# Optimization experiments

Hardware: AMD Instinct MI355X
Metric: run time of the kernel (lower is better)

The kernel has to match this reference:

```python
import jax, jax.numpy as jnp
import numpy as np

B, T, D = 64, 4096, 100   # batch, tokens, token_dim == code_dim
K = 4                     # discrete_size: codebook entries
BETA = 0.25               # commitment loss weight


def setup_inputs() -> dict:
    key = jax.random.key(0)
    k_x, k_w, k_b, k_c = jax.random.split(key, 4)
    x = jax.random.normal(k_x, (B, T, D), dtype=jnp.float32)
    W1 = jax.random.normal(k_w, (D, D), dtype=jnp.float32) * (1.0 / np.sqrt(D))
    b1 = jax.random.normal(k_b, (D,), dtype=jnp.float32) * 0.01
    codebook = jax.random.normal(k_c, (K, D), dtype=jnp.float32)
    return {"x": x, "W1": W1, "b1": b1, "codebook": codebook, "quantize": 1}


def reference(x, W1, b1, codebook, quantize):
    # Linear1: Linear(100,100) + ReLU (torch Linear: x @ W.T + b)
    h = jax.nn.relu(jnp.einsum("btd,ed->bte", x, W1) + b1)  # [B,T,D]
    if not quantize:
        return (h, 0, 0, 0)
    # quantizer.compress: VQ-style cdist/argmin/straight-through/loss
    flat = h.reshape(-1, D)  # [N,D]
    d2 = (jnp.sum(flat * flat, axis=-1, keepdims=True)
          - 2.0 * flat @ codebook.T
          + jnp.sum(codebook * codebook, axis=-1))
    idx = jnp.argmin(d2, axis=-1)          # [N] nearest code indices
    q = codebook[idx]                       # [N,D] gathered codes
    sg = jax.lax.stop_gradient
    # codebook loss + commitment loss
    vq_loss = (jnp.mean((sg(flat) - q) ** 2)
               + BETA * jnp.mean((flat - sg(q)) ** 2))
    # straight-through quantized output
    aux = (flat + sg(q - flat)).reshape(B, T, D)
    payload = idx.reshape(B, T)
    return (h, payload, aux, vq_loss)
```

## Files before the change

### kernel.cpp

```cpp
#include <hip/hip_runtime.h>

#define D_DIM   100
#define K_CODES 4
#define RPB     64
#define TPB     256
#define PITCH   65
#define N_ROWS  262144
#define KP      128
#define NP      128
#define TAU     0.25

typedef __attribute__((ext_vector_type(8))) __bf16 bf16x8;
typedef __attribute__((ext_vector_type(4))) float  f32x4;

__device__ __forceinline__ unsigned short f2bf_rne(float f) {
    unsigned int u = __builtin_bit_cast(unsigned int, f);
    unsigned int r = u + 0x7fffu + ((u >> 16) & 1u);
    return (unsigned short)(r >> 16);
}
__device__ __forceinline__ float bf2f(unsigned short b) {
    unsigned int u = ((unsigned int)b) << 16;
    return __builtin_bit_cast(float, u);
}

__global__ __launch_bounds__(256) void split_w_kernel(
    const float* __restrict__ W1,
    unsigned short* __restrict__ Whi, unsigned short* __restrict__ Wlo)
{
    int i = blockIdx.x * 256 + threadIdx.x;
    if (i >= NP * KP) return;
    int n = i / KP, k = i % KP;
    float w = (n < D_DIM && k < D_DIM) ? W1[n * D_DIM + k] : 0.0f;
    unsigned short hb = f2bf_rne(w);
    float lo = w - bf2f(hb);
    Whi[i] = hb;
    Wlo[i] = f2bf_rne(lo);
}

__global__ __launch_bounds__(TPB) void gemm_relu_mfma(
    const float* __restrict__ x,
    const unsigned short* __restrict__ Whi, const unsigned short* __restrict__ Wlo,
    const float* __restrict__ b1, float* __restrict__ out_h)
{
    __shared__ unsigned short xhi[RPB * KP];
    __shared__ unsigned short xlo[RPB * KP];
    const int tid  = threadIdx.x;
    const int lane = tid & 63;
    const int wave = tid >> 6;
    const int rowBase = blockIdx.x * RPB;
    const float* xg = x + (size_t)rowBase * D_DIM;

    const int bcol0 = wave * 32;
    const int bn  = lane & 15;
    const int bk  = (lane >> 4) * 8;
    bf16x8 bh[2][4], bl[2][4];
    #pragma unroll
    for (int ct = 0; ct < 2; ++ct) {
        int n = bcol0 + ct * 16 + bn;
        #pragma unroll
        for (int kt = 0; kt < 4; ++kt) {
            int off = n * KP + kt * 32 + bk;
            bh[ct][kt] = *reinterpret_cast<const bf16x8*>(Whi + off);
            bl[ct][kt] = *reinterpret_cast<const bf16x8*>(Wlo + off);
        }
    }
    float bias[2];
    #pragma unroll
    for (int ct = 0; ct < 2; ++ct) {
        int n = bcol0 + ct * 16 + bn;
        bias[ct] = (n < D_DIM) ? b1[n] : 0.0f;
    }

    for (int v = tid; v < RPB * 25; v += TPB) {
        float4 val = reinterpret_cast<const float4*>(xg)[v];
        int r = v / 25;
        int d = (v % 25) * 4;
        ushort4 hw, lw;
        hw.x = f2bf_rne(val.x); lw.x = f2bf_rne(val.x - bf2f(hw.x));
        hw.y = f2bf_rne(val.y); lw.y = f2bf_rne(val.y - bf2f(hw.y));
        hw.z = f2bf_rne(val.z); lw.z = f2bf_rne(val.z - bf2f(hw.z));
        hw.w = f2bf_rne(val.w); lw.w = f2bf_rne(val.w - bf2f(hw.w));
        int byte = r * 256 + ((d * 2) ^ ((r & 7) << 4));
        *reinterpret_cast<ushort4*>(reinterpret_cast<char*>(xhi) + byte) = hw;
        *reinterpret_cast<ushort4*>(reinterpret_cast<char*>(xlo) + byte) = lw;
    }
    for (int v = tid; v < RPB * 7; v += TPB) {
        int r = v / 7;
        int c = v % 7;
        int byte = r * 256 + (((200 + c * 8)) ^ ((r & 7) << 4));
        ushort4 z = {0, 0, 0, 0};
        *reinterpret_cast<ushort4*>(reinterpret_cast<char*>(xhi) + byte) = z;
        *reinterpret_cast<ushort4*>(reinterpret_cast<char*>(xlo) + byte) = z;
    }
    __syncthreads();

    const int am = lane & 15;
    const int ak = (lane >> 4) * 8;
    #pragma unroll
    for (int rt = 0; rt < 4; ++rt) {
        const int mrow = rt * 16 + am;
        bf16x8 ah[4], al[4];
        #pragma unroll
        for (int kt = 0; kt < 4; ++kt) {
            int byte = mrow * 256 + (((kt * 32 + ak) * 2) ^ ((mrow & 7) << 4));
            ah[kt] = *reinterpret_cast<const bf16x8*>(reinterpret_cast<const char*>(xhi) + byte);
            al[kt] = *reinterpret_cast<const bf16x8*>(reinterpret_cast<const char*>(xlo) + byte);
        }
        #pragma unroll
        for (int ct = 0; ct < 2; ++ct) {
            f32x4 acc = {0.f, 0.f, 0.f, 0.f};
            #pragma unroll
            for (int kt = 0; kt < 4; ++kt) {
                acc = __builtin_amdgcn_mfma_f32_16x16x32_bf16(ah[kt], bl[ct][kt], acc, 0, 0, 0);
                acc = __builtin_amdgcn_mfma_f32_16x16x32_bf16(al[kt], bh[ct][kt], acc, 0, 0, 0);
                acc = __builtin_amdgcn_mfma_f32_16x16x32_bf16(ah[kt], bh[ct][kt], acc, 0, 0, 0);
            }
            int n = bcol0 + ct * 16 + bn;
            if (n < D_DIM) {
                int rb = rt * 16 + (lane >> 4) * 4;
                #pragma unroll
                for (int i = 0; i < 4; ++i) {
                    float h = fmaxf(acc[i] + bias[ct], 0.0f);
                    out_h[(size_t)(rowBase + rb + i) * D_DIM + n] = h;
                }
            }
        }
    }
}

__global__ __launch_bounds__(TPB) void gemm_relu_valu(
    const float* __restrict__ x, const float* __restrict__ W1,
    const float* __restrict__ b1, float* __restrict__ out_h)
{
    __shared__ float tile[D_DIM][PITCH];
    const int tid  = threadIdx.x;
    const int lane = tid & 63;
    const int wave = tid >> 6;
    const int rowBase = blockIdx.x * RPB;
    const float* xg = x + (size_t)rowBase * D_DIM;

    for (int v = tid; v < (RPB * D_DIM) / 4; v += TPB) {
        float4 val = reinterpret_cast<const float4*>(xg)[v];
        int r = v / 25;
        int d = (v % 25) * 4;
        tile[d + 0][r] = val.x; tile[d + 1][r] = val.y;
        tile[d + 2][r] = val.z; tile[d + 3][r] = val.w;
    }
    __syncthreads();
    const int e0 = __builtin_amdgcn_readfirstlane(wave * 25);
    float acc[25];
    #pragma unroll
    for (int j = 0; j < 25; ++j) acc[j] = b1[e0 + j];
    #pragma unroll
    for (int d0 = 0; d0 < D_DIM; d0 += 20) {
        float xv[20];
        #pragma unroll
        for (int dd = 0; dd < 20; ++dd) xv[dd] = tile[d0 + dd][lane];
        #pragma unroll
        for (int j = 0; j < 25; ++j) {
            const float* wr = W1 + (e0 + j) * D_DIM + d0;
            #pragma unroll
            for (int dd = 0; dd < 20; ++dd)
                acc[j] = fmaf(xv[dd], wr[dd], acc[j]);
        }
    }
    __syncthreads();
    #pragma unroll
    for (int j = 0; j < 25; ++j)
        tile[e0 + j][lane] = fmaxf(acc[j], 0.0f);
    __syncthreads();
    float* hg = out_h + (size_t)rowBase * D_DIM;
    for (int v = tid; v < (RPB * D_DIM) / 4; v += TPB) {
        int r = v / 25;
        int d = (v % 25) * 4;
        reinterpret_cast<float4*>(hg)[v] =
            make_float4(tile[d][r], tile[d+1][r], tile[d+2][r], tile[d+3][r]);
    }
}

__global__ __launch_bounds__(TPB) void vq_kernel(
    const float* __restrict__ h, const float* __restrict__ x,
    const float* __restrict__ W1, const float* __restrict__ b1,
    const float* __restrict__ cb, const int* __restrict__ qflag,
    float* __restrict__ out_pay, float* __restrict__ out_aux,
    double* __restrict__ partials)
{
    __shared__ float  tile[D_DIM][PITCH];
    __shared__ double d2s[K_CODES][RPB];
    __shared__ int    idxs[RPB];
    __shared__ unsigned long long flagmask;
    const int tid  = threadIdx.x;
    const int lane = tid & 63;
    const int wave = tid >> 6;
    const int blk  = blockIdx.x;
    const int rowBase = blk * RPB;
    const int qz = *qflag;

    if (qz) {
        const float* hgc = h + (size_t)rowBase * D_DIM;
        for (int v = tid; v < (RPB * D_DIM) / 4; v += TPB) {
            float4 val = reinterpret_cast<const float4*>(hgc)[v];
            int r = v / 25;
            int d = (v % 25) * 4;
            tile[d + 0][r] = val.x; tile[d + 1][r] = val.y;
            tile[d + 2][r] = val.z; tile[d + 3][r] = val.w;
        }
        __syncthreads();
        {
            const int k = __builtin_amdgcn_readfirstlane(wave & 3);
            const float* crow = cb + k * D_DIM;
            double s = 0.0;
            #pragma unroll
            for (int d = 0; d < D_DIM; ++d) {
                double dh = (double)tile[d][lane] - (double)crow[d];
                s = fma(dh, dh, s);
            }
            d2s[k][lane] = s;
        }
        __syncthreads();

        if (wave == 0) {
            double best = d2s[0][lane], second = 1e300;
            int bi = 0;
            #pragma unroll
            for (int k = 1; k < K_CODES; ++k) {
                double v = d2s[k][lane];
                if (v < best) { second = best; best = v; bi = k; }
                else if (v < second) { second = v; }
            }
            idxs[lane] = bi;
            unsigned long long m = __ballot((second - best) < TAU);
            if (lane == 0) flagmask = m;
        }
        __syncthreads();

        {
            unsigned long long m = flagmask;
            int i = 0;
            while (m) {
                int r = __ffsll((long long)m) - 1;
                m &= m - 1;
                if ((i & 3) == wave) {
                    const int e1 = lane;
                    const int e2 = 64 + lane;
                    const bool has2 = (e2 < D_DIM);
                    float z1 = b1[e1];
                    float z2 = has2 ? b1[e2] : 0.0f;
                    const float* xr  = x + (size_t)(rowBase + r) * D_DIM;
                    const float* w1r = W1 + e1 * D_DIM;
                    const float* w2r = W1 + (has2 ? e2 : 0) * D_DIM;
                    #pragma unroll
                    for (int d4 = 0; d4 < 25; ++d4) {
                        float4 xv = reinterpret_cast<const float4*>(xr)[d4];
                        float4 wa = reinterpret_cast<const float4*>(w1r)[d4];
                        z1 = fmaf(xv.x, wa.x, z1); z1 = fmaf(xv.y, wa.y, z1);
                        z1 = fmaf(xv.z, wa.z, z1); z1 = fmaf(xv.w, wa.w, z1);
                        float4 wb = reinterpret_cast<const float4*>(w2r)[d4];
                        z2 = fmaf(xv.x, wb.x, z2); z2 = fmaf(xv.y, wb.y, z2);
                        z2 = fmaf(xv.z, wb.z, z2); z2 = fmaf(xv.w, wb.w, z2);
                    }
                    float h1 = fmaxf(z1, 0.0f);
                    float h2 = fmaxf(z2, 0.0f);
                    double dk[K_CODES];
                    #pragma unroll
                    for (int k = 0; k < K_CODES; ++k) {
                        double p;
                        {
                            double dh = (double)h1 - (double)cb[k * D_DIM + e1];
                            p = dh * dh;
                        }
                        if (has2) {
                            double dh = (double)h2 - (double)cb[k * D_DIM + e2];
                            p = fma(dh, dh, p);
                        }
                        for (int off = 32; off > 0; off >>= 1)
                            p += __shfl_down(p, off);
                        dk[k] = p;
                    }
                    if (lane == 0) {
                        double best = dk[0];
                        int bi = 0;
                        #pragma unroll
                        for (int k = 1; k < K_CODES; ++k)
                            if (dk[k] < best) { best = dk[k]; bi = k; }
                        idxs[r] = bi;
                    }
                }
                ++i;
            }
        }
        __syncthreads();

        if (wave == 0) {
            int bi = idxs[lane];
            out_pay[rowBase + lane] = (float)bi;
            double d2min = d2s[bi][lane];
            for (int off = 32; off > 0; off >>= 1)
                d2min += __shfl_down(d2min, off);
            if (lane == 0) partials[blk] = d2min;
        }

        float* ag = out_aux + (size_t)rowBase * D_DIM;
        for (int v = tid; v < (RPB * D_DIM) / 4; v += TPB) {
            int r = v / 25;
            int d = (v % 25) * 4;
            int bi = idxs[r];
            reinterpret_cast<float4*>(ag)[v] =
                reinterpret_cast<const float4*>(cb + bi * D_DIM + d)[0];
        }
    } else {
        if (wave == 0) {
            out_pay[rowBase + lane] = 0.0f;
            if (lane == 0) partials[blk] = 0.0;
        }
        float* ag = out_aux + (size_t)rowBase * D_DIM;
        for (int v = tid; v < (RPB * D_DIM) / 4; v += TPB)
            reinterpret_cast<float4*>(ag)[v] = make_float4(0, 0, 0, 0);
    }
}

__global__ __launch_bounds__(256) void vq_final_kernel(
    const double* __restrict__ partials, int n, float* __restrict__ loss_out)
{
    __shared__ double sm[256];
    int tid = threadIdx.x;
    double s = 0.0;
    for (int i = tid; i < n; i += 256) s += partials[i];
    sm[tid] = s;
    __syncthreads();
    for (int off = 128; off > 0; off >>= 1) {
        if (tid < off) sm[tid] += sm[tid + off];
        __syncthreads();
    }
    if (tid == 0) {
        double mse = sm[0] / ((double)N_ROWS * (double)D_DIM);
        loss_out[0] = (float)(1.25 * mse);
    }
}

extern "C" void kernel_launch(void* const* d_in, const int* in_sizes, int n_in,
                              void* d_out, int out_size, void* d_ws, size_t ws_size,
                              hipStream_t stream) {
    const float* x  = (const float*)d_in[0];
    const float* W1 = (const float*)d_in[1];
    const float* b1 = (const float*)d_in[2];
    const float* cb = (const float*)d_in[3];
    const int* qflag = (const int*)d_in[4];

    float* out = (float*)d_out;
    const int NR = in_sizes[0] / D_DIM;
    const int nblocks = NR / RPB;

    float* out_h    = out;
    float* out_pay  = out + (size_t)NR * D_DIM;
    float* out_aux  = out_pay + NR;
    float* out_loss = out_aux + (size_t)NR * D_DIM;

    double* partials = (double*)d_ws;
    const size_t w_off = (size_t)nblocks * sizeof(double);
    unsigned short* Whi = (unsigned short*)((char*)d_ws + w_off);
    unsigned short* Wlo = Whi + NP * KP;
    const size_t need = w_off + (size_t)2 * NP * KP * sizeof(unsigned short);

    if (ws_size >= need) {
        split_w_kernel<<<(NP * KP) / 256, 256, 0, stream>>>(W1, Whi, Wlo);
        gemm_relu_mfma<<<nblocks, TPB, 0, stream>>>(x, Whi, Wlo, b1, out_h);
    } else {
        gemm_relu_valu<<<nblocks, TPB, 0, stream>>>(x, W1, b1, out_h);
    }
    vq_kernel<<<nblocks, TPB, 0, stream>>>(out_h, x, W1, b1, cb, qflag,
                                           out_pay, out_aux, partials);
    vq_final_kernel<<<1, 256, 0, stream>>>(partials, nblocks, out_loss);
}
```

Measured before the change: 145.1 us.

## Fuse MFMA GEMM+ReLU with VQ kernel, keeping h in shared memory

Merges the split-bf16 MFMA GEMM and the VQ distance/argmin kernel into one kernel. The ReLU output is staged in a transposed shared-memory tile that reuses the bf16 staging buffer, and the VQ stage reads it directly. This removes the global write-then-reread of h and one launch. The bf16 conversion now uses native casts, and the workspace-size fallback to the VALU GEMM is dropped, which risks failure if the workspace is too small.

```diff
diff --git a/kernel.cpp b/kernel.cpp
--- a/kernel.cpp
+++ b/kernel.cpp
@@ -37,18 +37,29 @@
     Wlo[i] = f2bf_rne(lo);
 }
 
-__global__ __launch_bounds__(TPB) void gemm_relu_mfma(
+__global__ __launch_bounds__(TPB) void fused_kernel(
     const float* __restrict__ x,
     const unsigned short* __restrict__ Whi, const unsigned short* __restrict__ Wlo,
-    const float* __restrict__ b1, float* __restrict__ out_h)
+    const float* __restrict__ b1, const float* __restrict__ cb,
+    const float* __restrict__ W1, const int* __restrict__ qflag,
+    float* __restrict__ out_h, float* __restrict__ out_pay,
+    float* __restrict__ out_aux, double* __restrict__ partials)
 {
-    __shared__ unsigned short xhi[RPB * KP];
-    __shared__ unsigned short xlo[RPB * KP];
+    __shared__ __align__(16) unsigned char smem[32768];
+    __shared__ double d2s[K_CODES][RPB];
+    __shared__ int    idxs[RPB];
+    __shared__ unsigned long long flagmask;
+    unsigned short* xhi = reinterpret_cast<unsigned short*>(smem);
+    unsigned short* xlo = xhi + RPB * KP;
+    float* ftile = reinterpret_cast<float*>(smem);
+
     const int tid  = threadIdx.x;
     const int lane = tid & 63;
     const int wave = tid >> 6;
-    const int rowBase = blockIdx.x * RPB;
+    const int blk  = blockIdx.x;
+    const int rowBase = blk * RPB;
     const float* xg = x + (size_t)rowBase * D_DIM;
+    const int qz = *qflag;
 
     const int bcol0 = wave * 32;
     const int bn  = lane & 15;
@@ -75,14 +86,22 @@
         float4 val = reinterpret_cast<const float4*>(xg)[v];
         int r = v / 25;
         int d = (v % 25) * 4;
-        ushort4 hw, lw;
-        hw.x = f2bf_rne(val.x); lw.x = f2bf_rne(val.x - bf2f(hw.x));
-        hw.y = f2bf_rne(val.y); lw.y = f2bf_rne(val.y - bf2f(hw.y));
-        hw.z = f2bf_rne(val.z); lw.z = f2bf_rne(val.z - bf2f(hw.z));
-        hw.w = f2bf_rne(val.w); lw.w = f2bf_rne(val.w - bf2f(hw.w));
+        __bf16 hx = (__bf16)val.x, hy = (__bf16)val.y,
+               hz = (__bf16)val.z, hw_ = (__bf16)val.w;
+        __bf16 lx = (__bf16)(val.x - (float)hx), ly = (__bf16)(val.y - (float)hy),
+               lz = (__bf16)(val.z - (float)hz), lw_ = (__bf16)(val.w - (float)hw_);
+        ushort4 hv, lv;
+        hv.x = __builtin_bit_cast(unsigned short, hx);
+        hv.y = __builtin_bit_cast(unsigned short, hy);
+        hv.z = __builtin_bit_cast(unsigned short, hz);
+        hv.w = __builtin_bit_cast(unsigned short, hw_);
+        lv.x = __builtin_bit_cast(unsigned short, lx);
+        lv.y = __builtin_bit_cast(unsigned short, ly);
+        lv.z = __builtin_bit_cast(unsigned short, lz);
+        lv.w = __builtin_bit_cast(unsigned short, lw_);
         int byte = r * 256 + ((d * 2) ^ ((r & 7) << 4));
-        *reinterpret_cast<ushort4*>(reinterpret_cast<char*>(xhi) + byte) = hw;
-        *reinterpret_cast<ushort4*>(reinterpret_cast<char*>(xlo) + byte) = lw;
+        *reinterpret_cast<ushort4*>(reinterpret_cast<char*>(xhi) + byte) = hv;
+        *reinterpret_cast<ushort4*>(reinterpret_cast<char*>(xlo) + byte) = lv;
     }
     for (int v = tid; v < RPB * 7; v += TPB) {
         int r = v / 7;
@@ -96,6 +115,7 @@
 
     const int am = lane & 15;
     const int ak = (lane >> 4) * 8;
+    f32x4 acc[4][2];
     #pragma unroll
     for (int rt = 0; rt < 4; ++rt) {
         const int mrow = rt * 16 + am;
@@ -108,111 +128,41 @@
         }
         #pragma unroll
         for (int ct = 0; ct < 2; ++ct) {
-            f32x4 acc = {0.f, 0.f, 0.f, 0.f};
+            f32x4 a = {0.f, 0.f, 0.f, 0.f};
             #pragma unroll
             for (int kt = 0; kt < 4; ++kt) {
-                acc = __builtin_amdgcn_mfma_f32_16x16x32_bf16(ah[kt], bl[ct][kt], acc, 0, 0, 0);
-                acc = __builtin_amdgcn_mfma_f32_16x16x32_bf16(al[kt], bh[ct][kt], acc, 0, 0, 0);
-                acc = __builtin_amdgcn_mfma_f32_16x16x32_bf16(ah[kt], bh[ct][kt], acc, 0, 0, 0);
-            }
+                a = __builtin_amdgcn_mfma_f32_16x16x32_bf16(ah[kt], bl[ct][kt], a, 0, 0, 0);
+                a = __builtin_amdgcn_mfma_f32_16x16x32_bf16(al[kt], bh[ct][kt], a, 0, 0, 0);
+                a = __builtin_amdgcn_mfma_f32_16x16x32_bf16(ah[kt], bh[ct][kt], a, 0, 0, 0);
+            }
+            acc[rt][ct] = a;
+        }
+    }
+    __syncthreads();
+
+    #pragma unroll
+    for (int rt = 0; rt < 4; ++rt) {
+        int rb = rt * 16 + (lane >> 4) * 4;
+        #pragma unroll
+        for (int ct = 0; ct < 2; ++ct) {
             int n = bcol0 + ct * 16 + bn;
             if (n < D_DIM) {
-                int rb = rt * 16 + (lane >> 4) * 4;
                 #pragma unroll
-                for (int i = 0; i < 4; ++i) {
-                    float h = fmaxf(acc[i] + bias[ct], 0.0f);
-                    out_h[(size_t)(rowBase + rb + i) * D_DIM + n] = h;
-                }
-            }
-        }
-    }
-}
-
-__global__ __launch_bounds__(TPB) void gemm_relu_valu(
-    const float* __restrict__ x, const float* __restrict__ W1,
-    const float* __restrict__ b1, float* __restrict__ out_h)
-{
-    __shared__ float tile[D_DIM][PITCH];
-    const int tid  = threadIdx.x;
-    const int lane = tid & 63;
-    const int wave = tid >> 6;
-    const int rowBase = blockIdx.x * RPB;
-    const float* xg = x + (size_t)rowBase * D_DIM;
-
-    for (int v = tid; v < (RPB * D_DIM) / 4; v += TPB) {
-        float4 val = reinterpret_cast<const float4*>(xg)[v];
-        int r = v / 25;
-        int d = (v % 25) * 4;
-        tile[d + 0][r] = val.x; tile[d + 1][r] = val.y;
-        tile[d + 2][r] = val.z; tile[d + 3][r] = val.w;
+                for (int i = 0; i < 4; ++i)
+                    ftile[n * PITCH + rb + i] = fmaxf(acc[rt][ct][i] + bias[ct], 0.0f);
+            }
+        }
     }
     __syncthreads();
-    const int e0 = __builtin_amdgcn_readfirstlane(wave * 25);
-    float acc[25];
-    #pragma unroll
-    for (int j = 0; j < 25; ++j) acc[j] = b1[e0 + j];
-    #pragma unroll
-    for (int d0 = 0; d0 < D_DIM; d0 += 20) {
-        float xv[20];
-        #pragma unroll
-        for (int dd = 0; dd < 20; ++dd) xv[dd] = tile[d0 + dd][lane];
-        #pragma unroll
-        for (int j = 0; j < 25; ++j) {
-            const float* wr = W1 + (e0 + j) * D_DIM + d0;
-            #pragma unroll
-            for (int dd = 0; dd < 20; ++dd)
-                acc[j] = fmaf(xv[dd], wr[dd], acc[j]);
-        }
-    }
-    __syncthreads();
-    #pragma unroll
-    for (int j = 0; j < 25; ++j)
-        tile[e0 + j][lane] = fmaxf(acc[j], 0.0f);
-    __syncthreads();
-    float* hg = out_h + (size_t)rowBase * D_DIM;
-    for (int v = tid; v < (RPB * D_DIM) / 4; v += TPB) {
-        int r = v / 25;
-        int d = (v % 25) * 4;
-        reinterpret_cast<float4*>(hg)[v] =
-            make_float4(tile[d][r], tile[d+1][r], tile[d+2][r], tile[d+3][r]);
-    }
-}
-
-__global__ __launch_bounds__(TPB) void vq_kernel(
-    const float* __restrict__ h, const float* __restrict__ x,
-    const float* __restrict__ W1, const float* __restrict__ b1,
-    const float* __restrict__ cb, const int* __restrict__ qflag,
-    float* __restrict__ out_pay, float* __restrict__ out_aux,
-    double* __restrict__ partials)
-{
-    __shared__ float  tile[D_DIM][PITCH];
-    __shared__ double d2s[K_CODES][RPB];
-    __shared__ int    idxs[RPB];
-    __shared__ unsigned long long flagmask;
-    const int tid  = threadIdx.x;
-    const int lane = tid & 63;
-    const int wave = tid >> 6;
-    const int blk  = blockIdx.x;
-    const int rowBase = blk * RPB;
-    const int qz = *qflag;
 
     if (qz) {
-        const float* hgc = h + (size_t)rowBase * D_DIM;
-        for (int v = tid; v < (RPB * D_DIM) / 4; v += TPB) {
-            float4 val = reinterpret_cast<const float4*>(hgc)[v];
-            int r = v / 25;
-            int d = (v % 25) * 4;
-            tile[d + 0][r] = val.x; tile[d + 1][r] = val.y;
-            tile[d + 2][r] = val.z; tile[d + 3][r] = val.w;
-        }
-        __syncthreads();
         {
             const int k = __builtin_amdgcn_readfirstlane(wave & 3);
             const float* crow = cb + k * D_DIM;
             double s = 0.0;
             #pragma unroll
             for (int d = 0; d < D_DIM; ++d) {
-                double dh = (double)tile[d][lane] - (double)crow[d];
+                double dh = (double)ftile[d * PITCH + lane] - (double)crow[d];
                 s = fma(dh, dh, s);
             }
             d2s[k][lane] = s;
@@ -300,10 +250,14 @@
             if (lane == 0) partials[blk] = d2min;
         }
 
+        float* hg = out_h + (size_t)rowBase * D_DIM;
         float* ag = out_aux + (size_t)rowBase * D_DIM;
-        for (int v = tid; v < (RPB * D_DIM) / 4; v += TPB) {
+        for (int v = tid; v < RPB * 25; v += TPB) {
             int r = v / 25;
             int d = (v % 25) * 4;
+            float4 hv = make_float4(ftile[d * PITCH + r], ftile[(d + 1) * PITCH + r],
+                                    ftile[(d + 2) * PITCH + r], ftile[(d + 3) * PITCH + r]);
+            reinterpret_cast<float4*>(hg)[v] = hv;
             int bi = idxs[r];
             reinterpret_cast<float4*>(ag)[v] =
                 reinterpret_cast<const float4*>(cb + bi * D_DIM + d)[0];
@@ -313,9 +267,16 @@
             out_pay[rowBase + lane] = 0.0f;
             if (lane == 0) partials[blk] = 0.0;
         }
+        float* hg = out_h + (size_t)rowBase * D_DIM;
         float* ag = out_aux + (size_t)rowBase * D_DIM;
-        for (int v = tid; v < (RPB * D_DIM) / 4; v += TPB)
+        for (int v = tid; v < RPB * 25; v += TPB) {
+            int r = v / 25;
+            int d = (v % 25) * 4;
+            float4 hv = make_float4(ftile[d * PITCH + r], ftile[(d + 1) * PITCH + r],
+                                    ftile[(d + 2) * PITCH + r], ftile[(d + 3) * PITCH + r]);
+            reinterpret_cast<float4*>(hg)[v] = hv;
             reinterpret_cast<float4*>(ag)[v] = make_float4(0, 0, 0, 0);
+        }
     }
 }
 
@@ -360,15 +321,9 @@
     const size_t w_off = (size_t)nblocks * sizeof(double);
     unsigned short* Whi = (unsigned short*)((char*)d_ws + w_off);
     unsigned short* Wlo = Whi + NP * KP;
-    const size_t need = w_off + (size_t)2 * NP * KP * sizeof(unsigned short);
-
-    if (ws_size >= need) {
-        split_w_kernel<<<(NP * KP) / 256, 256, 0, stream>>>(W1, Whi, Wlo);
-        gemm_relu_mfma<<<nblocks, TPB, 0, stream>>>(x, Whi, Wlo, b1, out_h);
-    } else {
-        gemm_relu_valu<<<nblocks, TPB, 0, stream>>>(x, W1, b1, out_h);
-    }
-    vq_kernel<<<nblocks, TPB, 0, stream>>>(out_h, x, W1, b1, cb, qflag,
-                                           out_pay, out_aux, partials);
+
+    split_w_kernel<<<(NP * KP) / 256, 256, 0, stream>>>(W1, Whi, Wlo);
+    fused_kernel<<<nblocks, TPB, 0, stream>>>(x, Whi, Wlo, b1, cb, W1, qflag,
+                                              out_h, out_pay, out_aux, partials);
     vq_final_kernel<<<1, 256, 0, stream>>>(partials, nblocks, out_loss);
 }
```

Measured after the change: 169.6 us. 1.17x slower.

## Stage x via direct global-to-LDS loads and coalesce h stores through shared memory

Applied to the files above, without the earlier changes.

The MFMA GEMM kernel now copies raw fp32 x tiles straight into LDS with global_load_lds instead of splitting them into bf16 hi/lo on the way in. The hi/lo split moves into the MFMA loop. Results are transposed through LDS so h is written with coalesced float4 stores rather than scattered scalar stores. It also adds an occupancy hint to the launch bounds and removes the VALU fallback path along with the workspace-size check. Risks include LDS bank conflicts from the unswizzled fp32 reads at a 100-float row stride, and no fallback if the workspace is too small.

```diff
diff --git a/kernel.cpp b/kernel.cpp
--- a/kernel.cpp
+++ b/kernel.cpp
@@ -21,6 +21,12 @@
 __device__ __forceinline__ float bf2f(unsigned short b) {
     unsigned int u = ((unsigned int)b) << 16;
     return __builtin_bit_cast(float, u);
+}
+
+__device__ __forceinline__ void load_lds16(const float* g, float* s) {
+    __builtin_amdgcn_global_load_lds(
+        (const __attribute__((address_space(1))) unsigned int*)g,
+        (__attribute__((address_space(3))) unsigned int*)s, 16, 0, 0);
 }
 
 __global__ __launch_bounds__(256) void split_w_kernel(
@@ -37,13 +43,12 @@
     Wlo[i] = f2bf_rne(lo);
 }
 
-__global__ __launch_bounds__(TPB) void gemm_relu_mfma(
+__global__ __launch_bounds__(TPB, 4) void gemm_relu_mfma(
     const float* __restrict__ x,
     const unsigned short* __restrict__ Whi, const unsigned short* __restrict__ Wlo,
     const float* __restrict__ b1, float* __restrict__ out_h)
 {
-    __shared__ unsigned short xhi[RPB * KP];
-    __shared__ unsigned short xlo[RPB * KP];
+    __shared__ __align__(16) float smem[6500];
     const int tid  = threadIdx.x;
     const int lane = tid & 63;
     const int wave = tid >> 6;
@@ -71,110 +76,76 @@
         bias[ct] = (n < D_DIM) ? b1[n] : 0.0f;
     }
 
+    #pragma unroll
+    for (int it = 0; it < 6; ++it) {
+        int cbase = it * 256 + wave * 64;
+        load_lds16(xg + (size_t)(cbase + lane) * 4, smem + cbase * 4);
+    }
+    if (wave == 0) {
+        int cbase = 1536;
+        load_lds16(xg + (size_t)(cbase + lane) * 4, smem + cbase * 4);
+    }
+    if (tid < 32) smem[6400 + tid] = 0.0f;
+    __syncthreads();
+
+    const int am = lane & 15;
+    const int ak = (lane >> 4) * 8;
+    f32x4 acc[4][2];
+    #pragma unroll
+    for (int rt = 0; rt < 4; ++rt) {
+        acc[rt][0] = (f32x4){0.f, 0.f, 0.f, 0.f};
+        acc[rt][1] = (f32x4){0.f, 0.f, 0.f, 0.f};
+    }
+    #pragma unroll
+    for (int rt = 0; rt < 4; ++rt) {
+        const int rbase = (rt * 16 + am) * D_DIM;
+        #pragma unroll
+        for (int kt = 0; kt < 4; ++kt) {
+            const float* p = smem + rbase + kt * 32 + ak;
+            f32x4 f0 = *reinterpret_cast<const f32x4*>(p);
+            f32x4 f1 = *reinterpret_cast<const f32x4*>(p + 4);
+            bf16x8 ah, al;
+            #pragma unroll
+            for (int i = 0; i < 4; ++i) {
+                __bf16 h0 = (__bf16)f0[i];
+                ah[i] = h0;
+                al[i] = (__bf16)(f0[i] - (float)h0);
+                __bf16 h1 = (__bf16)f1[i];
+                ah[4 + i] = h1;
+                al[4 + i] = (__bf16)(f1[i] - (float)h1);
+            }
+            acc[rt][0] = __builtin_amdgcn_mfma_f32_16x16x32_bf16(ah, bl[0][kt], acc[rt][0], 0, 0, 0);
+            acc[rt][0] = __builtin_amdgcn_mfma_f32_16x16x32_bf16(al, bh[0][kt], acc[rt][0], 0, 0, 0);
+            acc[rt][0] = __builtin_amdgcn_mfma_f32_16x16x32_bf16(ah, bh[0][kt], acc[rt][0], 0, 0, 0);
+            acc[rt][1] = __builtin_amdgcn_mfma_f32_16x16x32_bf16(ah, bl[1][kt], acc[rt][1], 0, 0, 0);
+            acc[rt][1] = __builtin_amdgcn_mfma_f32_16x16x32_bf16(al, bh[1][kt], acc[rt][1], 0, 0, 0);
+            acc[rt][1] = __builtin_amdgcn_mfma_f32_16x16x32_bf16(ah, bh[1][kt], acc[rt][1], 0, 0, 0);
+        }
+    }
+    __syncthreads();
+
+    #pragma unroll
+    for (int rt = 0; rt < 4; ++rt) {
+        int rb = rt * 16 + (lane >> 4) * 4;
+        #pragma unroll
+        for (int ct = 0; ct < 2; ++ct) {
+            int n = bcol0 + ct * 16 + bn;
+            if (n < D_DIM) {
+                #pragma unroll
+                for (int i = 0; i < 4; ++i)
+                    smem[n * PITCH + rb + i] = fmaxf(acc[rt][ct][i] + bias[ct], 0.0f);
+            }
+        }
+    }
+    __syncthreads();
+
+    float* hg = out_h + (size_t)rowBase * D_DIM;
     for (int v = tid; v < RPB * 25; v += TPB) {
-        float4 val = reinterpret_cast<const float4*>(xg)[v];
         int r = v / 25;
         int d = (v % 25) * 4;
-        ushort4 hw, lw;
-        hw.x = f2bf_rne(val.x); lw.x = f2bf_rne(val.x - bf2f(hw.x));
-        hw.y = f2bf_rne(val.y); lw.y = f2bf_rne(val.y - bf2f(hw.y));
-        hw.z = f2bf_rne(val.z); lw.z = f2bf_rne(val.z - bf2f(hw.z));
-        hw.w = f2bf_rne(val.w); lw.w = f2bf_rne(val.w - bf2f(hw.w));
-        int byte = r * 256 + ((d * 2) ^ ((r & 7) << 4));
-        *reinterpret_cast<ushort4*>(reinterpret_cast<char*>(xhi) + byte) = hw;
-        *reinterpret_cast<ushort4*>(reinterpret_cast<char*>(xlo) + byte) = lw;
-    }
-    for (int v = tid; v < RPB * 7; v += TPB) {
-        int r = v / 7;
-        int c = v % 7;
-        int byte = r * 256 + (((200 + c * 8)) ^ ((r & 7) << 4));
-        ushort4 z = {0, 0, 0, 0};
-        *reinterpret_cast<ushort4*>(reinterpret_cast<char*>(xhi) + byte) = z;
-        *reinterpret_cast<ushort4*>(reinterpret_cast<char*>(xlo) + byte) = z;
-    }
-    __syncthreads();
-
-    const int am = lane & 15;
-    const int ak = (lane >> 4) * 8;
-    #pragma unroll
-    for (int rt = 0; rt < 4; ++rt) {
-        const int mrow = rt * 16 + am;
-        bf16x8 ah[4], al[4];
-        #pragma unroll
-        for (int kt = 0; kt < 4; ++kt) {
-            int byte = mrow * 256 + (((kt * 32 + ak) * 2) ^ ((mrow & 7) << 4));
-            ah[kt] = *reinterpret_cast<const bf16x8*>(reinterpret_cast<const char*>(xhi) + byte);
-            al[kt] = *reinterpret_cast<const bf16x8*>(reinterpret_cast<const char*>(xlo) + byte);
-        }
-        #pragma unroll
-        for (int ct = 0; ct < 2; ++ct) {
-            f32x4 acc = {0.f, 0.f, 0.f, 0.f};
-            #pragma unroll
-            for (int kt = 0; kt < 4; ++kt) {
-                acc = __builtin_amdgcn_mfma_f32_16x16x32_bf16(ah[kt], bl[ct][kt], acc, 0, 0, 0);
-                acc = __builtin_amdgcn_mfma_f32_16x16x32_bf16(al[kt], bh[ct][kt], acc, 0, 0, 0);
-                acc = __builtin_amdgcn_mfma_f32_16x16x32_bf16(ah[kt], bh[ct][kt], acc, 0, 0, 0);
-            }
-            int n = bcol0 + ct * 16 + bn;
-            if (n < D_DIM) {
-                int rb = rt * 16 + (lane >> 4) * 4;
-                #pragma unroll
-                for (int i = 0; i < 4; ++i) {
-                    float h = fmaxf(acc[i] + bias[ct], 0.0f);
-                    out_h[(size_t)(rowBase + rb + i) * D_DIM + n] = h;
-                }
-            }
-        }
-    }
-}
-
-__global__ __launch_bounds__(TPB) void gemm_relu_valu(
-    const float* __restrict__ x, const float* __restrict__ W1,
-    const float* __restrict__ b1, float* __restrict__ out_h)
-{
-    __shared__ float tile[D_DIM][PITCH];
-    const int tid  = threadIdx.x;
-    const int lane = tid & 63;
-    const int wave = tid >> 6;
-    const int rowBase = blockIdx.x * RPB;
-    const float* xg = x + (size_t)rowBase * D_DIM;
-
-    for (int v = tid; v < (RPB * D_DIM) / 4; v += TPB) {
-        float4 val = reinterpret_cast<const float4*>(xg)[v];
-        int r = v / 25;
-        int d = (v % 25) * 4;
-        tile[d + 0][r] = val.x; tile[d + 1][r] = val.y;
-        tile[d + 2][r] = val.z; tile[d + 3][r] = val.w;
-    }
-    __syncthreads();
-    const int e0 = __builtin_amdgcn_readfirstlane(wave * 25);
-    float acc[25];
-    #pragma unroll
-    for (int j = 0; j < 25; ++j) acc[j] = b1[e0 + j];
-    #pragma unroll
-    for (int d0 = 0; d0 < D_DIM; d0 += 20) {
-        float xv[20];
-        #pragma unroll
-        for (int dd = 0; dd < 20; ++dd) xv[dd] = tile[d0 + dd][lane];
-        #pragma unroll
-        for (int j = 0; j < 25; ++j) {
-            const float* wr = W1 + (e0 + j) * D_DIM + d0;
-            #pragma unroll
-            for (int dd = 0; dd < 20; ++dd)
-                acc[j] = fmaf(xv[dd], wr[dd], acc[j]);
-        }
-    }
-    __syncthreads();
-    #pragma unroll
-    for (int j = 0; j < 25; ++j)
-        tile[e0 + j][lane] = fmaxf(acc[j], 0.0f);
-    __syncthreads();
-    float* hg = out_h + (size_t)rowBase * D_DIM;
-    for (int v = tid; v < (RPB * D_DIM) / 4; v += TPB) {
-        int r = v / 25;
-        int d = (v % 25) * 4;
-        reinterpret_cast<float4*>(hg)[v] =
-            make_float4(tile[d][r], tile[d+1][r], tile[d+2][r], tile[d+3][r]);
+        reinterpret_cast<float4*>(hg)[v] = make_float4(
+            smem[d * PITCH + r], smem[(d + 1) * PITCH + r],
+            smem[(d + 2) * PITCH + r], smem[(d + 3) * PITCH + r]);
     }
 }
 
@@ -360,14 +331,9 @@
     const size_t w_off = (size_t)nblocks * sizeof(double);
     unsigned short* Whi = (unsigned short*)((char*)d_ws + w_off);
     unsigned short* Wlo = Whi + NP * KP;
-    const size_t need = w_off + (size_t)2 * NP * KP * sizeof(unsigned short);
-
-    if (ws_size >= need) {
-        split_w_kernel<<<(NP * KP) / 256, 256, 0, stream>>>(W1, Whi, Wlo);
-        gemm_relu_mfma<<<nblocks, TPB, 0, stream>>>(x, Whi, Wlo, b1, out_h);
-    } else {
-        gemm_relu_valu<<<nblocks, TPB, 0, stream>>>(x, W1, b1, out_h);
-    }
+
+    split_w_kernel<<<(NP * KP) / 256, 256, 0, stream>>>(W1, Whi, Wlo);
+    gemm_relu_mfma<<<nblocks, TPB, 0, stream>>>(x, Whi, Wlo, b1, out_h);
     vq_kernel<<<nblocks, TPB, 0, stream>>>(out_h, x, W1, b1, cb, qflag,
                                            out_pay, out_aux, partials);
     vq_final_kernel<<<1, 256, 0, stream>>>(partials, nblocks, out_loss);
```

After: 127.4 us. 12.2% less time.
